# Optimization experiments

Hardware: AMD Instinct MI355X
Metric: run time of the kernel (lower is better)

Reference implementation:

```python
import jax, jax.numpy as jnp
import numpy as np

HIDDEN = 2048
HEADS = 16
HEAD_DIM = HIDDEN // HEADS  # 128
ROPE_THETA = 10000.0


def rope_tables(L, d, theta, dtype=jnp.float32):
    inv_freq = 1.0 / (theta ** (jnp.arange(0, d, 2, dtype=jnp.float32) / d))  # [d/2]
    pos = jnp.arange(L, dtype=jnp.float32)
    freqs = pos[:, None] * inv_freq[None, :]            # [L, d/2]
    emb = jnp.concatenate([freqs, freqs], axis=-1)      # [L, d]
    return jnp.cos(emb).astype(dtype), jnp.sin(emb).astype(dtype)


def rotate_half(x):
    x1, x2 = jnp.split(x, 2, axis=-1)
    return jnp.concatenate([-x2, x1], axis=-1)


def setup_inputs() -> dict:
    key = jax.random.key(0)
    k1, k2, k3, k4, k5 = jax.random.split(key, 5)
    N, L = 2, 2048
    scale = 1.0 / np.sqrt(HIDDEN)
    return {
        "x": jax.random.normal(k1, (N, L, HIDDEN), dtype=jnp.float32),
        "wq": jax.random.normal(k2, (HIDDEN, HIDDEN), dtype=jnp.float32) * scale,
        "wk": jax.random.normal(k3, (HIDDEN, HIDDEN), dtype=jnp.float32) * scale,
        "wv": jax.random.normal(k4, (HIDDEN, HIDDEN), dtype=jnp.float32) * scale,
        "wo": jax.random.normal(k5, (HIDDEN, HIDDEN), dtype=jnp.float32) * scale,
    }


def reference(x, wq, wk, wv, wo):
    N, L, D = x.shape
    # QKV projections (torch Linear: y = x @ W.T)
    q = (x @ wq.T).reshape(N, L, HEADS, HEAD_DIM)
    k = (x @ wk.T).reshape(N, L, HEADS, HEAD_DIM)
    v = (x @ wv.T).reshape(N, L, HEADS, HEAD_DIM)
    # RoPE, broadcast over head dim (unsqueeze_dim=2)
    cos, sin = rope_tables(L, HEAD_DIM, ROPE_THETA, x.dtype)
    cos = cos[None, :, None, :]  # [1, L, 1, d]
    sin = sin[None, :, None, :]
    q = q * cos + rotate_half(q) * sin
    k = k * cos + rotate_half(k) * sin
    # causal SDPA over [N, H, L, d]
    scores = jnp.einsum("blhd,bmhd->bhlm", q, k) / jnp.sqrt(jnp.asarray(HEAD_DIM, x.dtype))
    causal = jnp.tril(jnp.ones((L, L), dtype=bool))
    scores = jnp.where(causal[None, None], scores, jnp.asarray(-jnp.inf, x.dtype))
    attn = jax.nn.softmax(scores, axis=-1)
    o = jnp.einsum("bhlm,bmhd->blhd", attn, v).reshape(N, L, D)
    return o @ wo.T
```

## Files before the change

### kernel.cpp

```cpp
#include <hip/hip_runtime.h>
#include <math.h>


typedef __bf16 bf16x8 __attribute__((ext_vector_type(8)));
typedef __bf16 bf16x4 __attribute__((ext_vector_type(4)));
typedef float  f32x4  __attribute__((ext_vector_type(4)));

#define AS1 __attribute__((address_space(1)))
#define AS3 __attribute__((address_space(3)))

static __device__ __forceinline__ void async_copy16(const void* g, void* l) {
  __builtin_amdgcn_global_load_lds((AS1 void*)g, (AS3 void*)l, 16, 0, 0);
}

__global__ __launch_bounds__(256) void cvt_all(
    const float* __restrict__ x,  const float* __restrict__ wq,
    const float* __restrict__ wk, const float* __restrict__ wv,
    const float* __restrict__ wo,
    __bf16* __restrict__ xb,  __bf16* __restrict__ wqb,
    __bf16* __restrict__ wkb, __bf16* __restrict__ wvb,
    __bf16* __restrict__ wob) {
  int i = blockIdx.x * 256 + threadIdx.x;
  const float* in; __bf16* out; int off;
  if (i < 2097152)      { in = x;  out = xb;  off = i; }
  else if (i < 3145728) { in = wq; out = wqb; off = i - 2097152; }
  else if (i < 4194304) { in = wk; out = wkb; off = i - 3145728; }
  else if (i < 5242880) { in = wv; out = wvb; off = i - 4194304; }
  else                  { in = wo; out = wob; off = i - 5242880; }
  float4 v = ((const float4*)in)[off];
  bf16x4 o;
  o[0] = (__bf16)v.x; o[1] = (__bf16)v.y; o[2] = (__bf16)v.z; o[3] = (__bf16)v.w;
  ((bf16x4*)out)[off] = o;
}

template <typename EpiF>
static __device__ __forceinline__ void gemm_body(const __bf16* __restrict__ A,
                                                 const __bf16* __restrict__ B,
                                                 int bm, int bn, EpiF&& epi) {
  constexpr int Kd = 2048;
  __shared__ __bf16 As[128 * 32];
  __shared__ __bf16 Bs[128 * 32];
  const int tid  = threadIdx.x;
  const int lane = tid & 63;
  const int wave = tid >> 6;
  const int l15 = lane & 15, l4 = lane >> 4;
  const int wm = (wave >> 1) * 64, wn = (wave & 1) * 64;

  const __bf16* Ag = A + (size_t)(bm + (tid >> 2)) * Kd + (tid & 3) * 8;
  const __bf16* Bg = B + (size_t)(bn + (tid >> 2)) * Kd + (tid & 3) * 8;
  __bf16* Asw = As + wave * 512;
  __bf16* Bsw = Bs + wave * 512;

  f32x4 acc[4][4] = {};

  for (int k0 = 0; k0 < Kd; k0 += 32) {
    async_copy16(Ag + k0, Asw);
    async_copy16(Ag + (size_t)64 * Kd + k0, Asw + 2048);
    async_copy16(Bg + k0, Bsw);
    async_copy16(Bg + (size_t)64 * Kd + k0, Bsw + 2048);
    __syncthreads();
    bf16x8 af[4], bfr[4];
#pragma unroll
    for (int i = 0; i < 4; ++i)
      af[i] = *(const bf16x8*)&As[(wm + 16 * i + l15) * 32 + 8 * l4];
#pragma unroll
    for (int j = 0; j < 4; ++j)
      bfr[j] = *(const bf16x8*)&Bs[(wn + 16 * j + l15) * 32 + 8 * l4];
#pragma unroll
    for (int i = 0; i < 4; ++i)
#pragma unroll
      for (int j = 0; j < 4; ++j)
        acc[i][j] = __builtin_amdgcn_mfma_f32_16x16x32_bf16(af[i], bfr[j], acc[i][j], 0, 0, 0);
    __syncthreads();
  }

#pragma unroll
  for (int i = 0; i < 4; ++i) {
    const int grow0 = bm + wm + 16 * i + 4 * l4;
#pragma unroll
    for (int j = 0; j < 4; ++j) {
      const int gcol = bn + wn + 16 * j + l15;
      epi(grow0, gcol, acc[i][j]);
    }
  }
}

__global__ __launch_bounds__(256) void gemm_qkv(const __bf16* __restrict__ A,
                                                const __bf16* __restrict__ wqb,
                                                const __bf16* __restrict__ wkb,
                                                const __bf16* __restrict__ wvb,
                                                __bf16* __restrict__ Qb,
                                                __bf16* __restrict__ Kb,
                                                __bf16* __restrict__ Vt) {
  const int z = blockIdx.z;
  const __bf16* B = (z == 0) ? wqb : (z == 1) ? wkb : wvb;
  const int bm = blockIdx.x * 128, bn = blockIdx.y * 128;
  if (z < 2) {
    __bf16* C = (z == 0) ? Qb : Kb;
    gemm_body(A, B, bm, bn, [&](int grow0, int gcol, const f32x4& a) {
#pragma unroll
      for (int r = 0; r < 4; ++r)
        C[(size_t)(grow0 + r) * 2048 + gcol] = (__bf16)a[r];
    });
  } else {
    gemm_body(A, B, bm, bn, [&](int grow0, int gcol, const f32x4& a) {
      const int b = grow0 >> 11, ll = grow0 & 2047;
      bf16x4 pk;
#pragma unroll
      for (int r = 0; r < 4; ++r) pk[r] = (__bf16)a[r];
      *(bf16x4*)(Vt + ((size_t)(b * 2048 + gcol)) * 2048 + ll) = pk;
    });
  }
}

__global__ __launch_bounds__(256) void gemm_out(const __bf16* __restrict__ A,
                                                const __bf16* __restrict__ B,
                                                float* __restrict__ C) {
  const int bm = blockIdx.x * 128, bn = blockIdx.y * 128;
  gemm_body(A, B, bm, bn, [&](int grow0, int gcol, const f32x4& a) {
#pragma unroll
    for (int r = 0; r < 4; ++r)
      C[(size_t)(grow0 + r) * 2048 + gcol] = a[r];
  });
}

__global__ __launch_bounds__(256) void rope_qk(__bf16* __restrict__ Q, __bf16* __restrict__ K) {
  const int t = blockIdx.x * 256 + threadIdx.x;
  const int d = t & 63;
  const int h = (t >> 6) & 15;
  const int row = t >> 10;
  const int pos = row & 2047;
  const size_t base = (size_t)row * 2048 + h * 128 + d;
  const float f = exp2f((float)d * (-13.287712379549449f / 64.0f));
  float s, c;
  sincosf((float)pos * f, &s, &c);
  const float qs = 0.08838834764831845f;
  float q1 = (float)Q[base], q2 = (float)Q[base + 64];
  Q[base]      = (__bf16)((q1 * c - q2 * s) * qs);
  Q[base + 64] = (__bf16)((q2 * c + q1 * s) * qs);
  float k1 = (float)K[base], k2 = (float)K[base + 64];
  K[base]      = (__bf16)(k1 * c - k2 * s);
  K[base + 64] = (__bf16)(k2 * c + k1 * s);
}

__global__ __launch_bounds__(256) void attn_flash(const __bf16* __restrict__ Q,
                                                  const __bf16* __restrict__ Km,
                                                  const __bf16* __restrict__ Vt,
                                                  __bf16* __restrict__ O) {
  __shared__ __bf16 Ks[2][4096];
  __shared__ __bf16 Vs[2][4096];
  __shared__ __bf16 Pl[4][512];
  const int lane = threadIdx.x & 63;
  const int wave = threadIdx.x >> 6;
  const int l15 = lane & 15, l4 = lane >> 4;

  const int id = blockIdx.x;
  const int xcd = id & 7, j = id >> 3;
  const int g = j >> 5;
  const int bh = xcd + 8 * g;
  const int qb = ((j & 31) + 8 * g) & 31;
  const int qbase = qb * 64;
  const int b = bh >> 4, h = bh & 15;
  const int qw = qbase + wave * 16;

  const int srow = lane >> 2;
  const int sc   = lane & 3;
  const __bf16* Kg0 = Km + ((size_t)(b * 2048 + srow)) * 2048 + h * 128 + wave * 32 + sc * 8;
  const __bf16* Vg0 = Vt + ((size_t)(b * 2048 + h * 128 + wave * 32 + srow)) * 2048 + sc * 8;

  const __bf16* Qbase = Q + ((size_t)(b * 2048 + qw + l15)) * 2048 + h * 128 + 8 * l4;
  bf16x8 aq[4];
#pragma unroll
  for (int st = 0; st < 4; ++st) aq[st] = *(const bf16x8*)(Qbase + st * 32);

  bf16x8 ones;
#pragma unroll
  for (int jj = 0; jj < 8; ++jj) ones[jj] = (__bf16)1.0f;

  f32x4 oa[8] = {};
  f32x4 os = {};

  const int nkb = qbase / 32 + 2;

  {
    async_copy16(Kg0,                      &Ks[0][wave * 1024]);
    async_copy16(Kg0 + (size_t)16 * 2048,  &Ks[0][wave * 1024 + 512]);
    async_copy16(Vg0,                      &Vs[0][wave * 1024]);
    async_copy16(Vg0 + (size_t)16 * 2048,  &Vs[0][wave * 1024 + 512]);
  }

  for (int kb = 0; kb < nkb; ++kb) {
    const int buf = kb & 1;
    __syncthreads();
    if (kb + 1 < nkb) {
      const size_t koff = (size_t)(kb + 1) * 32 * 2048;
      const int nb = buf ^ 1;
      async_copy16(Kg0 + koff,                     &Ks[nb][wave * 1024]);
      async_copy16(Kg0 + koff + (size_t)16 * 2048, &Ks[nb][wave * 1024 + 512]);
      async_copy16(Vg0 + (kb + 1) * 32,            &Vs[nb][wave * 1024]);
      async_copy16(Vg0 + (kb + 1) * 32 + (size_t)16 * 2048, &Vs[nb][wave * 1024 + 512]);
    }
    const int kpos = kb * 32;

    f32x4 s[2] = {};
#pragma unroll
    for (int nt = 0; nt < 2; ++nt)
#pragma unroll
      for (int st = 0; st < 4; ++st) {
        bf16x8 bk = *(const bf16x8*)&Ks[buf][st * 1024 + (nt * 16 + l15) * 32 + 8 * l4];
        s[nt] = __builtin_amdgcn_mfma_f32_16x16x32_bf16(aq[st], bk, s[nt], 0, 0, 0);
      }

    const bool diag = (kpos + 31 > qw);
    __bf16* pw = &Pl[wave][0];
#pragma unroll
    for (int nt = 0; nt < 2; ++nt) {
      const int col = kpos + nt * 16 + l15;
#pragma unroll
      for (int r = 0; r < 4; ++r) {
        float p = __expf(fminf(s[nt][r], 40.f));
        if (diag && col > qw + 4 * l4 + r) p = 0.f;
        pw[(4 * l4 + r) * 32 + nt * 16 + l15] = (__bf16)p;
      }
    }
    bf16x8 ap = *(const bf16x8*)&pw[l15 * 32 + 8 * l4];
    os = __builtin_amdgcn_mfma_f32_16x16x32_bf16(ap, ones, os, 0, 0, 0);
#pragma unroll
    for (int dt = 0; dt < 8; ++dt) {
      bf16x8 bv = *(const bf16x8*)&Vs[buf][dt * 512 + l15 * 32 + 8 * l4];
      oa[dt] = __builtin_amdgcn_mfma_f32_16x16x32_bf16(ap, bv, oa[dt], 0, 0, 0);
    }
  }

  float inv[4];
#pragma unroll
  for (int r = 0; r < 4; ++r) inv[r] = 1.0f / os[r];

  __bf16* Obase = O + ((size_t)(b * 2048 + qw + 4 * l4)) * 2048 + h * 128;
#pragma unroll
  for (int dt = 0; dt < 8; ++dt)
#pragma unroll
    for (int r = 0; r < 4; ++r)
      Obase[(size_t)r * 2048 + dt * 16 + l15] = (__bf16)(oa[dt][r] * inv[r]);
}

extern "C" void kernel_launch(void* const* d_in, const int* in_sizes, int n_in,
                              void* d_out, int out_size, void* d_ws, size_t ws_size,
                              hipStream_t stream) {
  const float* x  = (const float*)d_in[0];
  const float* wq = (const float*)d_in[1];
  const float* wk = (const float*)d_in[2];
  const float* wv = (const float*)d_in[3];
  const float* wo = (const float*)d_in[4];

  char* ws = (char*)d_ws;
  __bf16* xb  = (__bf16*)(ws + 0);
  __bf16* wqb = (__bf16*)(ws + 16777216);
  __bf16* wkb = (__bf16*)(ws + 25165824);
  __bf16* wvb = (__bf16*)(ws + 33554432);
  __bf16* wob = (__bf16*)(ws + 41943040);
  __bf16* Qb  = (__bf16*)(ws + 50331648);
  __bf16* Kb  = (__bf16*)(ws + 67108864);
  __bf16* Vt  = (__bf16*)(ws + 83886080);
  __bf16* Ob  = xb;

  cvt_all<<<24576, 256, 0, stream>>>(x, wq, wk, wv, wo, xb, wqb, wkb, wvb, wob);

  gemm_qkv<<<dim3(32, 16, 3), 256, 0, stream>>>(xb, wqb, wkb, wvb, Qb, Kb, Vt);

  rope_qk<<<16384, 256, 0, stream>>>(Qb, Kb);

  attn_flash<<<1024, 256, 0, stream>>>(Qb, Kb, Vt, Ob);

  gemm_out<<<dim3(32, 16), 256, 0, stream>>>(Ob, wob, (float*)d_out);
}
```

Before: 399.2 us.

## Fuse RoPE into QKV GEMM epilogue and double query rows per attention block

The GEMM warp tiling is remapped so each wave holds both halves (d and d+64) of a head's columns, letting RoPE and the query scale be applied in the Q/K projection epilogue. This removes the separate rope_qk kernel and its extra read-modify-write pass over Q and K. Separately, each attention wave now processes 32 query rows (two 16-row MFMA tiles) against each loaded K/V tile, halving the grid to 512 blocks and reusing K/V loads across twice as many queries. The trade-offs are more registers per wave, fewer blocks in flight, and coarser causal load balancing.

```diff
diff --git a/kernel.cpp b/kernel.cpp
--- a/kernel.cpp
+++ b/kernel.cpp
@@ -33,10 +33,9 @@
   ((bf16x4*)out)[off] = o;
 }
 
-template <typename EpiF>
-static __device__ __forceinline__ void gemm_body(const __bf16* __restrict__ A,
+static __device__ __forceinline__ void gemm_core(const __bf16* __restrict__ A,
                                                  const __bf16* __restrict__ B,
-                                                 int bm, int bn, EpiF&& epi) {
+                                                 int bm, int bn, f32x4 acc[4][4]) {
   constexpr int Kd = 2048;
   __shared__ __bf16 As[128 * 32];
   __shared__ __bf16 Bs[128 * 32];
@@ -44,14 +43,13 @@
   const int lane = tid & 63;
   const int wave = tid >> 6;
   const int l15 = lane & 15, l4 = lane >> 4;
-  const int wm = (wave >> 1) * 64, wn = (wave & 1) * 64;
+  const int wm = (wave >> 1) * 64;
+  const int cw = (wave & 1) * 32;
 
   const __bf16* Ag = A + (size_t)(bm + (tid >> 2)) * Kd + (tid & 3) * 8;
   const __bf16* Bg = B + (size_t)(bn + (tid >> 2)) * Kd + (tid & 3) * 8;
   __bf16* Asw = As + wave * 512;
   __bf16* Bsw = Bs + wave * 512;
-
-  f32x4 acc[4][4] = {};
 
   for (int k0 = 0; k0 < Kd; k0 += 32) {
     async_copy16(Ag + k0, Asw);
@@ -65,23 +63,13 @@
       af[i] = *(const bf16x8*)&As[(wm + 16 * i + l15) * 32 + 8 * l4];
 #pragma unroll
     for (int j = 0; j < 4; ++j)
-      bfr[j] = *(const bf16x8*)&Bs[(wn + 16 * j + l15) * 32 + 8 * l4];
+      bfr[j] = *(const bf16x8*)&Bs[(cw + (j & 1) * 16 + (j >> 1) * 64 + l15) * 32 + 8 * l4];
 #pragma unroll
     for (int i = 0; i < 4; ++i)
 #pragma unroll
       for (int j = 0; j < 4; ++j)
         acc[i][j] = __builtin_amdgcn_mfma_f32_16x16x32_bf16(af[i], bfr[j], acc[i][j], 0, 0, 0);
     __syncthreads();
-  }
-
-#pragma unroll
-  for (int i = 0; i < 4; ++i) {
-    const int grow0 = bm + wm + 16 * i + 4 * l4;
-#pragma unroll
-    for (int j = 0; j < 4; ++j) {
-      const int gcol = bn + wn + 16 * j + l15;
-      epi(grow0, gcol, acc[i][j]);
-    }
   }
 }
 
@@ -95,21 +83,55 @@
   const int z = blockIdx.z;
   const __bf16* B = (z == 0) ? wqb : (z == 1) ? wkb : wvb;
   const int bm = blockIdx.x * 128, bn = blockIdx.y * 128;
+  f32x4 acc[4][4] = {};
+  gemm_core(A, B, bm, bn, acc);
+
+  const int lane = threadIdx.x & 63;
+  const int wave = threadIdx.x >> 6;
+  const int l15 = lane & 15, l4 = lane >> 4;
+  const int wm = (wave >> 1) * 64;
+  const int cw = (wave & 1) * 32;
+
   if (z < 2) {
-    __bf16* C = (z == 0) ? Qb : Kb;
-    gemm_body(A, B, bm, bn, [&](int grow0, int gcol, const f32x4& a) {
-#pragma unroll
-      for (int r = 0; r < 4; ++r)
-        C[(size_t)(grow0 + r) * 2048 + gcol] = (__bf16)a[r];
-    });
+    __bf16* C = z ? Kb : Qb;
+    const float scale = z ? 1.0f : 0.08838834764831845f;
+    float fr[2];
+#pragma unroll
+    for (int jp = 0; jp < 2; ++jp) {
+      const int d = cw + jp * 16 + l15;
+      fr[jp] = exp2f((float)d * -0.20762050593045f);
+    }
+#pragma unroll
+    for (int i = 0; i < 4; ++i) {
+      const int grow0 = bm + wm + 16 * i + 4 * l4;
+#pragma unroll
+      for (int jp = 0; jp < 2; ++jp) {
+        const int gcol = bn + cw + jp * 16 + l15;
+#pragma unroll
+        for (int r = 0; r < 4; ++r) {
+          const int pos = (grow0 + r) & 2047;
+          const float th = (float)pos * fr[jp];
+          const float cv = __cosf(th), sv = __sinf(th);
+          const float a1 = acc[i][jp][r], a2 = acc[i][jp + 2][r];
+          C[(size_t)(grow0 + r) * 2048 + gcol]      = (__bf16)((a1 * cv - a2 * sv) * scale);
+          C[(size_t)(grow0 + r) * 2048 + gcol + 64] = (__bf16)((a2 * cv + a1 * sv) * scale);
+        }
+      }
+    }
   } else {
-    gemm_body(A, B, bm, bn, [&](int grow0, int gcol, const f32x4& a) {
-      const int b = grow0 >> 11, ll = grow0 & 2047;
-      bf16x4 pk;
-#pragma unroll
-      for (int r = 0; r < 4; ++r) pk[r] = (__bf16)a[r];
-      *(bf16x4*)(Vt + ((size_t)(b * 2048 + gcol)) * 2048 + ll) = pk;
-    });
+#pragma unroll
+    for (int i = 0; i < 4; ++i) {
+      const int grow0 = bm + wm + 16 * i + 4 * l4;
+      const int bb = grow0 >> 11, ll = grow0 & 2047;
+#pragma unroll
+      for (int j = 0; j < 4; ++j) {
+        const int gcol = bn + cw + (j & 1) * 16 + (j >> 1) * 64 + l15;
+        bf16x4 pk;
+#pragma unroll
+        for (int r = 0; r < 4; ++r) pk[r] = (__bf16)acc[i][j][r];
+        *(bf16x4*)(Vt + ((size_t)(bb * 2048 + gcol)) * 2048 + ll) = pk;
+      }
+    }
   }
 }
 
@@ -117,30 +139,24 @@
                                                 const __bf16* __restrict__ B,
                                                 float* __restrict__ C) {
   const int bm = blockIdx.x * 128, bn = blockIdx.y * 128;
-  gemm_body(A, B, bm, bn, [&](int grow0, int gcol, const f32x4& a) {
-#pragma unroll
-    for (int r = 0; r < 4; ++r)
-      C[(size_t)(grow0 + r) * 2048 + gcol] = a[r];
-  });
-}
-
-__global__ __launch_bounds__(256) void rope_qk(__bf16* __restrict__ Q, __bf16* __restrict__ K) {
-  const int t = blockIdx.x * 256 + threadIdx.x;
-  const int d = t & 63;
-  const int h = (t >> 6) & 15;
-  const int row = t >> 10;
-  const int pos = row & 2047;
-  const size_t base = (size_t)row * 2048 + h * 128 + d;
-  const float f = exp2f((float)d * (-13.287712379549449f / 64.0f));
-  float s, c;
-  sincosf((float)pos * f, &s, &c);
-  const float qs = 0.08838834764831845f;
-  float q1 = (float)Q[base], q2 = (float)Q[base + 64];
-  Q[base]      = (__bf16)((q1 * c - q2 * s) * qs);
-  Q[base + 64] = (__bf16)((q2 * c + q1 * s) * qs);
-  float k1 = (float)K[base], k2 = (float)K[base + 64];
-  K[base]      = (__bf16)(k1 * c - k2 * s);
-  K[base + 64] = (__bf16)(k2 * c + k1 * s);
+  f32x4 acc[4][4] = {};
+  gemm_core(A, B, bm, bn, acc);
+  const int lane = threadIdx.x & 63;
+  const int wave = threadIdx.x >> 6;
+  const int l15 = lane & 15, l4 = lane >> 4;
+  const int wm = (wave >> 1) * 64;
+  const int cw = (wave & 1) * 32;
+#pragma unroll
+  for (int i = 0; i < 4; ++i) {
+    const int grow0 = bm + wm + 16 * i + 4 * l4;
+#pragma unroll
+    for (int j = 0; j < 4; ++j) {
+      const int gcol = bn + cw + (j & 1) * 16 + (j >> 1) * 64 + l15;
+#pragma unroll
+      for (int r = 0; r < 4; ++r)
+        C[(size_t)(grow0 + r) * 2048 + gcol] = acc[i][j][r];
+    }
+  }
 }
 
 __global__ __launch_bounds__(256) void attn_flash(const __bf16* __restrict__ Q,
@@ -149,45 +165,45 @@
                                                   __bf16* __restrict__ O) {
   __shared__ __bf16 Ks[2][4096];
   __shared__ __bf16 Vs[2][4096];
-  __shared__ __bf16 Pl[4][512];
+  __shared__ __bf16 Pl[4][1024];
   const int lane = threadIdx.x & 63;
   const int wave = threadIdx.x >> 6;
   const int l15 = lane & 15, l4 = lane >> 4;
 
   const int id = blockIdx.x;
-  const int xcd = id & 7, j = id >> 3;
-  const int g = j >> 5;
+  const int xcd = id & 7, jj = id >> 3;
+  const int g = jj >> 4;
   const int bh = xcd + 8 * g;
-  const int qb = ((j & 31) + 8 * g) & 31;
-  const int qbase = qb * 64;
+  const int qb = ((jj & 15) + 4 * g) & 15;
+  const int qbase = qb * 128;
   const int b = bh >> 4, h = bh & 15;
-  const int qw = qbase + wave * 16;
-
-  const int srow = lane >> 2;
-  const int sc   = lane & 3;
+  const int qw0 = qbase + wave * 32;
+
+  const int srow = lane >> 2, sc = lane & 3;
   const __bf16* Kg0 = Km + ((size_t)(b * 2048 + srow)) * 2048 + h * 128 + wave * 32 + sc * 8;
   const __bf16* Vg0 = Vt + ((size_t)(b * 2048 + h * 128 + wave * 32 + srow)) * 2048 + sc * 8;
 
-  const __bf16* Qbase = Q + ((size_t)(b * 2048 + qw + l15)) * 2048 + h * 128 + 8 * l4;
-  bf16x8 aq[4];
-#pragma unroll
-  for (int st = 0; st < 4; ++st) aq[st] = *(const bf16x8*)(Qbase + st * 32);
+  bf16x8 aq[2][4];
+#pragma unroll
+  for (int m = 0; m < 2; ++m) {
+    const __bf16* Qb2 = Q + ((size_t)(b * 2048 + qw0 + 16 * m + l15)) * 2048 + h * 128 + 8 * l4;
+#pragma unroll
+    for (int st = 0; st < 4; ++st) aq[m][st] = *(const bf16x8*)(Qb2 + st * 32);
+  }
 
   bf16x8 ones;
 #pragma unroll
-  for (int jj = 0; jj < 8; ++jj) ones[jj] = (__bf16)1.0f;
-
-  f32x4 oa[8] = {};
-  f32x4 os = {};
-
-  const int nkb = qbase / 32 + 2;
-
-  {
-    async_copy16(Kg0,                      &Ks[0][wave * 1024]);
-    async_copy16(Kg0 + (size_t)16 * 2048,  &Ks[0][wave * 1024 + 512]);
-    async_copy16(Vg0,                      &Vs[0][wave * 1024]);
-    async_copy16(Vg0 + (size_t)16 * 2048,  &Vs[0][wave * 1024 + 512]);
-  }
+  for (int q = 0; q < 8; ++q) ones[q] = (__bf16)1.0f;
+
+  f32x4 oa[2][8] = {};
+  f32x4 os[2] = {};
+
+  const int nkb = qb * 4 + 4;
+
+  async_copy16(Kg0,                     &Ks[0][wave * 1024]);
+  async_copy16(Kg0 + (size_t)16 * 2048, &Ks[0][wave * 1024 + 512]);
+  async_copy16(Vg0,                     &Vs[0][wave * 1024]);
+  async_copy16(Vg0 + (size_t)16 * 2048, &Vs[0][wave * 1024 + 512]);
 
   for (int kb = 0; kb < nkb; ++kb) {
     const int buf = kb & 1;
@@ -195,53 +211,67 @@
     if (kb + 1 < nkb) {
       const size_t koff = (size_t)(kb + 1) * 32 * 2048;
       const int nb = buf ^ 1;
-      async_copy16(Kg0 + koff,                     &Ks[nb][wave * 1024]);
-      async_copy16(Kg0 + koff + (size_t)16 * 2048, &Ks[nb][wave * 1024 + 512]);
-      async_copy16(Vg0 + (kb + 1) * 32,            &Vs[nb][wave * 1024]);
+      async_copy16(Kg0 + koff,                      &Ks[nb][wave * 1024]);
+      async_copy16(Kg0 + koff + (size_t)16 * 2048,  &Ks[nb][wave * 1024 + 512]);
+      async_copy16(Vg0 + (kb + 1) * 32,             &Vs[nb][wave * 1024]);
       async_copy16(Vg0 + (kb + 1) * 32 + (size_t)16 * 2048, &Vs[nb][wave * 1024 + 512]);
     }
     const int kpos = kb * 32;
 
-    f32x4 s[2] = {};
+    f32x4 s[2][2] = {};
 #pragma unroll
     for (int nt = 0; nt < 2; ++nt)
 #pragma unroll
       for (int st = 0; st < 4; ++st) {
         bf16x8 bk = *(const bf16x8*)&Ks[buf][st * 1024 + (nt * 16 + l15) * 32 + 8 * l4];
-        s[nt] = __builtin_amdgcn_mfma_f32_16x16x32_bf16(aq[st], bk, s[nt], 0, 0, 0);
+#pragma unroll
+        for (int m = 0; m < 2; ++m)
+          s[m][nt] = __builtin_amdgcn_mfma_f32_16x16x32_bf16(aq[m][st], bk, s[m][nt], 0, 0, 0);
       }
 
-    const bool diag = (kpos + 31 > qw);
-    __bf16* pw = &Pl[wave][0];
-#pragma unroll
-    for (int nt = 0; nt < 2; ++nt) {
-      const int col = kpos + nt * 16 + l15;
-#pragma unroll
-      for (int r = 0; r < 4; ++r) {
-        float p = __expf(fminf(s[nt][r], 40.f));
-        if (diag && col > qw + 4 * l4 + r) p = 0.f;
-        pw[(4 * l4 + r) * 32 + nt * 16 + l15] = (__bf16)p;
+#pragma unroll
+    for (int m = 0; m < 2; ++m) {
+      const int qwm = qw0 + 16 * m;
+      const bool diag = (kpos + 31 > qwm);
+      __bf16* pw = &Pl[wave][m * 512];
+#pragma unroll
+      for (int nt = 0; nt < 2; ++nt) {
+        const int col = kpos + nt * 16 + l15;
+#pragma unroll
+        for (int r = 0; r < 4; ++r) {
+          float p = __expf(fminf(s[m][nt][r], 40.f));
+          if (diag && col > qwm + 4 * l4 + r) p = 0.f;
+          pw[(4 * l4 + r) * 32 + nt * 16 + l15] = (__bf16)p;
+        }
       }
     }
-    bf16x8 ap = *(const bf16x8*)&pw[l15 * 32 + 8 * l4];
-    os = __builtin_amdgcn_mfma_f32_16x16x32_bf16(ap, ones, os, 0, 0, 0);
+    bf16x8 ap[2];
+#pragma unroll
+    for (int m = 0; m < 2; ++m) {
+      ap[m] = *(const bf16x8*)&Pl[wave][m * 512 + l15 * 32 + 8 * l4];
+      os[m] = __builtin_amdgcn_mfma_f32_16x16x32_bf16(ap[m], ones, os[m], 0, 0, 0);
+    }
 #pragma unroll
     for (int dt = 0; dt < 8; ++dt) {
       bf16x8 bv = *(const bf16x8*)&Vs[buf][dt * 512 + l15 * 32 + 8 * l4];
-      oa[dt] = __builtin_amdgcn_mfma_f32_16x16x32_bf16(ap, bv, oa[dt], 0, 0, 0);
-    }
-  }
-
-  float inv[4];
-#pragma unroll
-  for (int r = 0; r < 4; ++r) inv[r] = 1.0f / os[r];
-
-  __bf16* Obase = O + ((size_t)(b * 2048 + qw + 4 * l4)) * 2048 + h * 128;
-#pragma unroll
-  for (int dt = 0; dt < 8; ++dt)
-#pragma unroll
-    for (int r = 0; r < 4; ++r)
-      Obase[(size_t)r * 2048 + dt * 16 + l15] = (__bf16)(oa[dt][r] * inv[r]);
+#pragma unroll
+      for (int m = 0; m < 2; ++m)
+        oa[m][dt] = __builtin_amdgcn_mfma_f32_16x16x32_bf16(ap[m], bv, oa[m][dt], 0, 0, 0);
+    }
+  }
+
+#pragma unroll
+  for (int m = 0; m < 2; ++m) {
+    float inv[4];
+#pragma unroll
+    for (int r = 0; r < 4; ++r) inv[r] = 1.0f / os[m][r];
+    __bf16* Obase = O + ((size_t)(b * 2048 + qw0 + 16 * m + 4 * l4)) * 2048 + h * 128;
+#pragma unroll
+    for (int dt = 0; dt < 8; ++dt)
+#pragma unroll
+      for (int r = 0; r < 4; ++r)
+        Obase[(size_t)r * 2048 + dt * 16 + l15] = (__bf16)(oa[m][dt][r] * inv[r]);
+  }
 }
 
 extern "C" void kernel_launch(void* const* d_in, const int* in_sizes, int n_in,
@@ -268,9 +298,7 @@
 
   gemm_qkv<<<dim3(32, 16, 3), 256, 0, stream>>>(xb, wqb, wkb, wvb, Qb, Kb, Vt);
 
-  rope_qk<<<16384, 256, 0, stream>>>(Qb, Kb);
-
-  attn_flash<<<1024, 256, 0, stream>>>(Qb, Kb, Vt, Ob);
+  attn_flash<<<512, 256, 0, stream>>>(Qb, Kb, Vt, Ob);
 
   gemm_out<<<dim3(32, 16), 256, 0, stream>>>(Ob, wob, (float*)d_out);
 }
```

New measurement: 389.3 us. -2.5%, faster.
